# Performance work log

Measured on AMD Instinct MI355X. Metric: run time of the kernel, lower is better.

The kernel has to match this reference:

```python
import jax, jax.numpy as jnp
import numpy as np

B, N, D = 2, 2048, 512
H, VD = 8, 64  # v_dim = hid_dim / n_head


def setup_inputs() -> dict:
    key = jax.random.key(0)
    k1, k2, k3, k4 = jax.random.split(key, 4)
    inputs = jax.random.normal(k1, (B, N, D), dtype=jnp.float32)
    # lecun_normal: std = 1/sqrt(fan_in) with fan_in = D
    s = 1.0 / np.sqrt(D)
    q_w = jax.random.normal(k2, (H, D, VD), dtype=jnp.float32) * s
    k_w = jax.random.normal(k3, (H, D, VD), dtype=jnp.float32) * s
    v_w = jax.random.normal(k4, (H, D, VD), dtype=jnp.float32) * s
    return {"inputs": inputs, "q_w": q_w, "k_w": k_w, "v_w": v_w}


def reference(inputs, q_w, k_w, v_w):
    # QKV projections: [B,N,D] x [H,D,VD] -> [B,H,N,VD]
    q = jnp.einsum('bnj,hjk->bhnk', inputs, q_w)
    k = jnp.einsum('bnj,hjk->bhnk', inputs, k_w)
    v = jnp.einsum('bnj,hjk->bhnk', inputs, v_w)
    scale = 1.0 / jnp.sqrt(jnp.asarray(VD, dtype=q.dtype))
    scores = jnp.einsum('bhik,bhjk->bhij', q, k) * scale  # [B,H,N,N]
    att = jax.nn.softmax(scores, axis=-1)
    out = jnp.einsum('bhnj,bhjd->bhnd', att, v)  # [B,H,N,VD]
    out = jnp.transpose(out, (0, 2, 1, 3)).reshape(inputs.shape[0], -1, H * VD)  # [B,N,hid_dim]
    # keras GELU default is exact (non-approximate)
    return jax.nn.gelu(out, approximate=False)
```

## Files before the change

kernel.cpp:

```cpp
#include <hip/hip_runtime.h>
#include <hip/hip_bf16.h>
#include <math.h>

#define BB 2
#define NN 2048
#define DD 512
#define HH 8
#define VD 64

typedef _Float16 half8 __attribute__((ext_vector_type(8)));
typedef _Float16 half4 __attribute__((ext_vector_type(4)));
typedef __fp16 fp16x2 __attribute__((ext_vector_type(2)));
typedef float f32x4 __attribute__((ext_vector_type(4)));

#define GLDS16(gp, lp) __builtin_amdgcn_global_load_lds( \
    (const __attribute__((address_space(1))) void*)(gp), \
    (__attribute__((address_space(3))) void*)(lp), 16, 0, 0)

__device__ __forceinline__ float fexp2(float x) {
#if __has_builtin(__builtin_amdgcn_exp2f)
    return __builtin_amdgcn_exp2f(x);
#else
    return exp2f(x);
#endif
}

__device__ __forceinline__ void stage8(const _Float16* gsrc, size_t ldg, int r0,
                                       _Float16* lbase, int lane) {
    int r8 = lane >> 3;
    int ce = ((lane & 7) ^ r8) << 3;
    const _Float16* g = gsrc + (size_t)(r0 + r8) * ldg + ce;
    GLDS16(g, lbase);
}

__device__ __forceinline__ half8 frag_ld(const _Float16* tile, int row, int cb) {
    int off = row * 128 + (cb ^ ((row & 7) << 4));
    return *(const half8*)((const char*)tile + off);
}

__device__ __forceinline__ half8 frag_ldv(const _Float16* tile, int row, int cb) {
    int off = row * 256 + (cb ^ ((row & 15) << 4));
    return *(const half8*)((const char*)tile + off);
}

__device__ __forceinline__ float gelu_exact(float v) {
    return 0.5f * v * (1.f + erff(v * 0.70710678118654752f));
}

__global__ __launch_bounds__(256) void prep_kernel(
    const float* __restrict__ x,
    const float* __restrict__ qw, const float* __restrict__ kw,
    const float* __restrict__ vw,
    _Float16* __restrict__ wt, _Float16* __restrict__ xh)
{
    __shared__ float ls[64][65];
    const int t = threadIdx.x;
    const int bid = blockIdx.x;
    if (bid < 192) {
        const int kc = bid & 7, h = (bid >> 3) & 7, ty = bid >> 6;
        const float* src = (ty == 0) ? qw : (ty == 1) ? kw : vw;
#pragma unroll
        for (int j = 0; j < 4; ++j) {
            int idx = t + 256 * j;
            int k = idx >> 4, o4 = idx & 15;
            float4 v = *(const float4*)(src + ((size_t)(h * DD + kc * 64 + k) * VD + o4 * 4));
            ls[k][o4 * 4 + 0] = v.x; ls[k][o4 * 4 + 1] = v.y;
            ls[k][o4 * 4 + 2] = v.z; ls[k][o4 * 4 + 3] = v.w;
        }
        __syncthreads();
#pragma unroll
        for (int j = 0; j < 4; ++j) {
            int idx = t + 256 * j;
            int o = idx >> 4, k4 = idx & 15;
            half4 hv;
#pragma unroll
            for (int i = 0; i < 4; ++i) hv[i] = (_Float16)ls[k4 * 4 + i][o];
            *(half4*)(wt + ((size_t)(ty * HH + h) * VD + o) * DD + kc * 64 + k4 * 4) = hv;
        }
    } else {
        size_t idx = ((size_t)(bid - 192) * 256 + t) * 8;
        float4 a = *(const float4*)(x + idx);
        float4 b = *(const float4*)(x + idx + 4);
        half8 hv;
        hv[0] = (_Float16)a.x; hv[1] = (_Float16)a.y;
        hv[2] = (_Float16)a.z; hv[3] = (_Float16)a.w;
        hv[4] = (_Float16)b.x; hv[5] = (_Float16)b.y;
        hv[6] = (_Float16)b.z; hv[7] = (_Float16)b.w;
        *(half8*)(xh + idx) = hv;
    }
}

__global__ __launch_bounds__(256) void qkv_proj_kernel(
    const _Float16* __restrict__ xh,
    const _Float16* __restrict__ wt,
    _Float16* __restrict__ qsp,
    _Float16* __restrict__ kbp,
    _Float16* __restrict__ vtp)
{
    __shared__ __align__(16) _Float16 xls[2][4096];
    __shared__ __align__(16) _Float16 wls[2][12288];
    const int t = threadIdx.x;
    const int wave = t >> 6, lane = t & 63;
    const int lq = lane & 15, g = lane >> 4;
    const int bid = blockIdx.x;
    const int h = bid & 7;
    const int m0 = (bid >> 3) * 64;
    const int rbase = 32 * (wave >> 1);
    const int cbase = 96 * (wave & 1);

    f32x4 acc[2][6];
#pragma unroll
    for (int a = 0; a < 2; ++a)
#pragma unroll
        for (int c = 0; c < 6; ++c) acc[a][c] = (f32x4){0.f, 0.f, 0.f, 0.f};

    auto stage = [&](int buf, int ks) {
#pragma unroll
        for (int j = 0; j < 2; ++j) {
            int i = wave * 2 + j;
            stage8(xh + (size_t)m0 * DD + ks * 64, DD, i * 8, &xls[buf][i * 512], lane);
        }
#pragma unroll
        for (int j = 0; j < 6; ++j) {
            int i = wave * 6 + j;
            int ty = i >> 3;
            int ol = (i & 7) * 8;
            stage8(wt + ((size_t)(ty * HH + h) * VD + ol) * DD + ks * 64, DD, 0,
                   &wls[buf][i * 512], lane);
        }
    };

    stage(0, 0);
    stage(1, 1);
    for (int ks = 0; ks < 8; ++ks) {
        const int buf = ks & 1;
        if (ks < 7) asm volatile("s_waitcnt vmcnt(8)" ::: "memory");
        else        asm volatile("s_waitcnt vmcnt(0)" ::: "memory");
        __builtin_amdgcn_s_barrier();
        half8 af[2][2];
        half8 bf[6][2];
#pragma unroll
        for (int amt = 0; amt < 2; ++amt) {
            af[amt][0] = frag_ld(xls[buf], rbase + amt * 16 + lq, 16 * g);
            af[amt][1] = frag_ld(xls[buf], rbase + amt * 16 + lq, 64 + 16 * g);
        }
#pragma unroll
        for (int ct = 0; ct < 6; ++ct) {
            int wr = cbase + ct * 16 + lq;
            bf[ct][0] = frag_ld(wls[buf], wr, 16 * g);
            bf[ct][1] = frag_ld(wls[buf], wr, 64 + 16 * g);
        }
        asm volatile("s_waitcnt lgkmcnt(0)" ::: "memory");
        __builtin_amdgcn_sched_barrier(0);
        __builtin_amdgcn_s_barrier();
        if (ks + 2 < 8) stage(buf, ks + 2);
        __builtin_amdgcn_s_setprio(1);
#pragma unroll
        for (int ct = 0; ct < 6; ++ct) {
#pragma unroll
            for (int amt = 0; amt < 2; ++amt) {
                acc[amt][ct] = __builtin_amdgcn_mfma_f32_16x16x32_f16(af[amt][0], bf[ct][0], acc[amt][ct], 0, 0, 0);
                acc[amt][ct] = __builtin_amdgcn_mfma_f32_16x16x32_f16(af[amt][1], bf[ct][1], acc[amt][ct], 0, 0, 0);
            }
        }
        __builtin_amdgcn_s_setprio(0);
    }

#pragma unroll
    for (int ct = 0; ct < 6; ++ct) {
        int gcol = cbase + ct * 16 + lq;
        int ty = gcol >> 6, o = gcol & 63;
#pragma unroll
        for (int amt = 0; amt < 2; ++amt) {
#pragma unroll
            for (int i = 0; i < 4; ++i) {
                int ng = m0 + rbase + amt * 16 + 4 * g + i;
                int b = ng >> 11, nb = ng & (NN - 1);
                size_t bh = (size_t)(b * HH + h);
                float v = acc[amt][ct][i];
                if (ty == 0)      qsp[(bh * NN + nb) * VD + o] = (_Float16)(v * 0.18033688011112042f);
                else if (ty == 1) kbp[(bh * NN + nb) * VD + o] = (_Float16)v;
                else {
                    int nbp = (nb & ~31) | (((nb >> 2) & 3) << 3) | (((nb >> 4) & 1) << 2) | (nb & 3);
                    vtp[(bh * VD + o) * NN + nbp] = (_Float16)v;
                }
            }
        }
    }
}

__global__ __launch_bounds__(256, 2) void attn_kernel(
    const _Float16* __restrict__ qs,
    const _Float16* __restrict__ kb,
    const _Float16* __restrict__ vt,
    float* __restrict__ out)
{
    constexpr int NITER = NN / 128;
    __shared__ __align__(16) char SM[65536 + 1024];
    const int t = threadIdx.x;
    const int wave = t >> 6, lane = t & 63;
    const int lq = lane & 15, g = lane >> 4;
    const int bid = blockIdx.x;
    const int xcd = bid & 7;
    const int bh = xcd * 2 + ((bid >> 3) & 1);
    const int qt = bid >> 4;
    const int qbase = qt * 64;

    half8 qf[4][2];
#pragma unroll
    for (int qg = 0; qg < 4; ++qg)
#pragma unroll
        for (int ds = 0; ds < 2; ++ds)
            qf[qg][ds] = *(const half8*)(qs + ((size_t)bh * NN + qbase + 16 * qg + lq) * VD + 32 * ds + 8 * g);

    const int r8 = lane >> 3;
    const _Float16* kS = kb + ((size_t)bh * NN + 32 * wave + r8) * VD + 8 * ((lane & 7) ^ r8);
    const _Float16* vS[4];
#pragma unroll
    for (int uu = 0; uu < 4; ++uu) {
        int vrow = 16 * wave + 4 * uu + g;
        vS[uu] = vt + ((size_t)bh * VD + vrow) * NN + 8 * (lq ^ (vrow & 15));
    }

    _Float16* kb0 = (_Float16*)(SM);
    _Float16* vb0 = (_Float16*)(SM + 16384);
    _Float16* kb1 = (_Float16*)(SM + 32768);
    _Float16* vb1 = (_Float16*)(SM + 49152);

    auto stage = [&](int b, int j) {
        _Float16* kd = (b ? kb1 : kb0) + 4 * wave * 512;
        const _Float16* kp = kS + (size_t)j * 128 * VD;
#pragma unroll
        for (int uu = 0; uu < 4; ++uu)
            GLDS16(kp + uu * 8 * VD, kd + uu * 512);
        _Float16* vd = (b ? vb1 : vb0) + 4 * wave * 512;
#pragma unroll
        for (int uu = 0; uu < 4; ++uu)
            GLDS16(vS[uu] + j * 128, vd + uu * 512);
    };

    f32x4 oacc[4][4];
#pragma unroll
    for (int qg = 0; qg < 4; ++qg)
#pragma unroll
        for (int dt = 0; dt < 4; ++dt) oacc[qg][dt] = (f32x4){0.f, 0.f, 0.f, 0.f};
    float lsum[4] = {0.f, 0.f, 0.f, 0.f};

    stage(0, 0);
    stage(1, 1);

    union PU { fp16x2 h2[4]; half8 h8; };

    for (int j = 0; j < NITER; ++j) {
        const int b = j & 1;
        if (j < NITER - 1) asm volatile("s_waitcnt vmcnt(8)" ::: "memory");
        else               asm volatile("s_waitcnt vmcnt(0)" ::: "memory");
        __builtin_amdgcn_s_barrier();
        const _Float16* kB = b ? kb1 : kb0;
        const _Float16* vB = b ? vb1 : vb0;
        half8 kf[2][2], vf[4];
#pragma unroll
        for (int mt = 0; mt < 2; ++mt)
#pragma unroll
            for (int ds = 0; ds < 2; ++ds)
                kf[mt][ds] = frag_ld(kB, 32 * wave + 16 * mt + lq, 64 * ds + 16 * g);
#pragma unroll
        for (int dt = 0; dt < 4; ++dt)
            vf[dt] = frag_ldv(vB, 16 * dt + lq, 64 * wave + 16 * g);
        asm volatile("s_waitcnt lgkmcnt(0)" ::: "memory");
        __builtin_amdgcn_sched_barrier(0);
        __builtin_amdgcn_s_barrier();
        if (j + 2 < NITER) stage(b, j + 2);
        f32x4 sacc[4][2];
        __builtin_amdgcn_s_setprio(1);
#pragma unroll
        for (int qg = 0; qg < 4; ++qg) {
#pragma unroll
            for (int mt = 0; mt < 2; ++mt) {
                f32x4 sv = (f32x4){0.f, 0.f, 0.f, 0.f};
                sv = __builtin_amdgcn_mfma_f32_16x16x32_f16(kf[mt][0], qf[qg][0], sv, 0, 0, 0);
                sv = __builtin_amdgcn_mfma_f32_16x16x32_f16(kf[mt][1], qf[qg][1], sv, 0, 0, 0);
                sacc[qg][mt] = sv;
            }
        }
        __builtin_amdgcn_s_setprio(0);
        PU pu[4];
#pragma unroll
        for (int qg = 0; qg < 4; ++qg) {
            float p00 = fexp2(sacc[qg][0][0]);
            float p01 = fexp2(sacc[qg][0][1]);
            float p02 = fexp2(sacc[qg][0][2]);
            float p03 = fexp2(sacc[qg][0][3]);
            float p10 = fexp2(sacc[qg][1][0]);
            float p11 = fexp2(sacc[qg][1][1]);
            float p12 = fexp2(sacc[qg][1][2]);
            float p13 = fexp2(sacc[qg][1][3]);
            lsum[qg] += ((p00 + p01) + (p02 + p03)) + ((p10 + p11) + (p12 + p13));
            pu[qg].h2[0] = __builtin_amdgcn_cvt_pkrtz(p00, p01);
            pu[qg].h2[1] = __builtin_amdgcn_cvt_pkrtz(p02, p03);
            pu[qg].h2[2] = __builtin_amdgcn_cvt_pkrtz(p10, p11);
            pu[qg].h2[3] = __builtin_amdgcn_cvt_pkrtz(p12, p13);
        }
        __builtin_amdgcn_s_setprio(1);
#pragma unroll
        for (int qg = 0; qg < 4; ++qg)
#pragma unroll
            for (int dt = 0; dt < 4; ++dt)
                oacc[qg][dt] = __builtin_amdgcn_mfma_f32_16x16x32_f16(vf[dt], pu[qg].h8, oacc[qg][dt], 0, 0, 0);
        __builtin_amdgcn_s_setprio(0);
    }

#pragma unroll
    for (int qg = 0; qg < 4; ++qg) {
        lsum[qg] += __shfl_xor(lsum[qg], 16, 64);
        lsum[qg] += __shfl_xor(lsum[qg], 32, 64);
    }
    float* lsm  = (float*)(SM + 65536);
    float* sred = (float*)SM;
    __syncthreads();
    if (g == 0) {
#pragma unroll
        for (int qg = 0; qg < 4; ++qg) lsm[wave * 64 + 16 * qg + lq] = lsum[qg];
    }
#pragma unroll
    for (int qg = 0; qg < 4; ++qg)
#pragma unroll
        for (int dt = 0; dt < 4; ++dt)
            *(f32x4*)(sred + (size_t)wave * 4096 + (16 * qg + lq) * 64 + 16 * dt + 4 * g) = oacc[qg][dt];
    __syncthreads();
    const int b2 = bh >> 3, h = bh & 7;
    const int q = t >> 2, cg = t & 3;
    float lt = (lsm[q] + lsm[64 + q]) + (lsm[128 + q] + lsm[192 + q]);
    float inv = 1.f / lt;
    float* op = out + ((size_t)b2 * NN + qbase + q) * (HH * VD) + h * VD + 16 * cg;
#pragma unroll
    for (int c2 = 0; c2 < 4; ++c2) {
        int off = q * 64 + 16 * cg + 4 * c2;
        f32x4 o = *(const f32x4*)(sred + off);
        o += *(const f32x4*)(sred + 4096 + off);
        o += *(const f32x4*)(sred + 8192 + off);
        o += *(const f32x4*)(sred + 12288 + off);
        float4 r;
        r.x = gelu_exact(o[0] * inv);
        r.y = gelu_exact(o[1] * inv);
        r.z = gelu_exact(o[2] * inv);
        r.w = gelu_exact(o[3] * inv);
        *(float4*)(op + 4 * c2) = r;
    }
}

extern "C" void kernel_launch(void* const* d_in, const int* in_sizes, int n_in,
                              void* d_out, int out_size, void* d_ws, size_t ws_size,
                              hipStream_t stream)
{
    const float* x  = (const float*)d_in[0];
    const float* qw = (const float*)d_in[1];
    const float* kw = (const float*)d_in[2];
    const float* vw = (const float*)d_in[3];
    float* out = (float*)d_out;

    _Float16* wt  = (_Float16*)d_ws;
    _Float16* xhp = wt  + 786432;
    _Float16* qsp = xhp + 2097152;
    _Float16* kbp = qsp + 2097152;
    _Float16* vtp = kbp + 2097152;

    hipLaunchKernelGGL(prep_kernel, dim3(192 + 1024), dim3(256), 0, stream,
                       x, qw, kw, vw, wt, xhp);
    hipLaunchKernelGGL(qkv_proj_kernel, dim3(512), dim3(256), 0, stream,
                       xhp, wt, qsp, kbp, vtp);
    hipLaunchKernelGGL(attn_kernel, dim3(512), dim3(256), 0, stream,
                       qsp, kbp, vtp, out);
}
```

Measured before the change: 53.21 us.

## Enlarge QKV projection row tile and interleave score/exp/PV in attention

The QKV projection kernel now handles 128 rows per block instead of 64, halving the grid and reusing each staged weight tile across twice as many rows, at the cost of more LDS and accumulator registers. The attention loop is restructured to software-pipeline per query group: the QK^T MFMAs for the next group are issued while exp and PV run for the current group, which shortens register lifetimes and overlaps transcendental work with matrix work. The row sum of probabilities is now computed by an extra MFMA against a vector of ones instead of scalar adds and cross-lane shuffles. This adds MFMA work and a larger per-block footprint in the projection, which may reduce occupancy.

```diff
diff --git a/kernel.cpp b/kernel.cpp
--- a/kernel.cpp
+++ b/kernel.cpp
@@ -90,34 +90,34 @@
     }
 }
 
-__global__ __launch_bounds__(256) void qkv_proj_kernel(
+__global__ __launch_bounds__(256, 1) void qkv_proj_kernel(
     const _Float16* __restrict__ xh,
     const _Float16* __restrict__ wt,
     _Float16* __restrict__ qsp,
     _Float16* __restrict__ kbp,
     _Float16* __restrict__ vtp)
 {
-    __shared__ __align__(16) _Float16 xls[2][4096];
+    __shared__ __align__(16) _Float16 xls[2][8192];
     __shared__ __align__(16) _Float16 wls[2][12288];
     const int t = threadIdx.x;
     const int wave = t >> 6, lane = t & 63;
     const int lq = lane & 15, g = lane >> 4;
     const int bid = blockIdx.x;
     const int h = bid & 7;
-    const int m0 = (bid >> 3) * 64;
-    const int rbase = 32 * (wave >> 1);
+    const int m0 = (bid >> 3) * 128;
+    const int rbase = 64 * (wave >> 1);
     const int cbase = 96 * (wave & 1);
 
-    f32x4 acc[2][6];
-#pragma unroll
-    for (int a = 0; a < 2; ++a)
+    f32x4 acc[4][6];
+#pragma unroll
+    for (int a = 0; a < 4; ++a)
 #pragma unroll
         for (int c = 0; c < 6; ++c) acc[a][c] = (f32x4){0.f, 0.f, 0.f, 0.f};
 
     auto stage = [&](int buf, int ks) {
 #pragma unroll
-        for (int j = 0; j < 2; ++j) {
-            int i = wave * 2 + j;
+        for (int j = 0; j < 4; ++j) {
+            int i = wave * 4 + j;
             stage8(xh + (size_t)m0 * DD + ks * 64, DD, i * 8, &xls[buf][i * 512], lane);
         }
 #pragma unroll
@@ -134,13 +134,13 @@
     stage(1, 1);
     for (int ks = 0; ks < 8; ++ks) {
         const int buf = ks & 1;
-        if (ks < 7) asm volatile("s_waitcnt vmcnt(8)" ::: "memory");
+        if (ks < 7) asm volatile("s_waitcnt vmcnt(10)" ::: "memory");
         else        asm volatile("s_waitcnt vmcnt(0)" ::: "memory");
         __builtin_amdgcn_s_barrier();
-        half8 af[2][2];
+        half8 af[4][2];
         half8 bf[6][2];
 #pragma unroll
-        for (int amt = 0; amt < 2; ++amt) {
+        for (int amt = 0; amt < 4; ++amt) {
             af[amt][0] = frag_ld(xls[buf], rbase + amt * 16 + lq, 16 * g);
             af[amt][1] = frag_ld(xls[buf], rbase + amt * 16 + lq, 64 + 16 * g);
         }
@@ -158,7 +158,7 @@
 #pragma unroll
         for (int ct = 0; ct < 6; ++ct) {
 #pragma unroll
-            for (int amt = 0; amt < 2; ++amt) {
+            for (int amt = 0; amt < 4; ++amt) {
                 acc[amt][ct] = __builtin_amdgcn_mfma_f32_16x16x32_f16(af[amt][0], bf[ct][0], acc[amt][ct], 0, 0, 0);
                 acc[amt][ct] = __builtin_amdgcn_mfma_f32_16x16x32_f16(af[amt][1], bf[ct][1], acc[amt][ct], 0, 0, 0);
             }
@@ -171,7 +171,7 @@
         int gcol = cbase + ct * 16 + lq;
         int ty = gcol >> 6, o = gcol & 63;
 #pragma unroll
-        for (int amt = 0; amt < 2; ++amt) {
+        for (int amt = 0; amt < 4; ++amt) {
 #pragma unroll
             for (int i = 0; i < 4; ++i) {
                 int ng = m0 + rbase + amt * 16 + 4 * g + i;
@@ -240,11 +240,16 @@
     };
 
     f32x4 oacc[4][4];
-#pragma unroll
-    for (int qg = 0; qg < 4; ++qg)
+    f32x4 oacc_l[4];
+#pragma unroll
+    for (int qg = 0; qg < 4; ++qg) {
 #pragma unroll
         for (int dt = 0; dt < 4; ++dt) oacc[qg][dt] = (f32x4){0.f, 0.f, 0.f, 0.f};
-    float lsum[4] = {0.f, 0.f, 0.f, 0.f};
+        oacc_l[qg] = (f32x4){0.f, 0.f, 0.f, 0.f};
+    }
+    half8 vones;
+#pragma unroll
+    for (int i = 0; i < 8; ++i) vones[i] = (_Float16)1.0f;
 
     stage(0, 0);
     stage(1, 1);
@@ -271,56 +276,54 @@
         __builtin_amdgcn_sched_barrier(0);
         __builtin_amdgcn_s_barrier();
         if (j + 2 < NITER) stage(b, j + 2);
-        f32x4 sacc[4][2];
+        f32x4 sc[2][2];
         __builtin_amdgcn_s_setprio(1);
 #pragma unroll
+        for (int mt = 0; mt < 2; ++mt) {
+            sc[0][mt] = (f32x4){0.f, 0.f, 0.f, 0.f};
+            sc[0][mt] = __builtin_amdgcn_mfma_f32_16x16x32_f16(kf[mt][0], qf[0][0], sc[0][mt], 0, 0, 0);
+            sc[0][mt] = __builtin_amdgcn_mfma_f32_16x16x32_f16(kf[mt][1], qf[0][1], sc[0][mt], 0, 0, 0);
+        }
+#pragma unroll
         for (int qg = 0; qg < 4; ++qg) {
-#pragma unroll
-            for (int mt = 0; mt < 2; ++mt) {
-                f32x4 sv = (f32x4){0.f, 0.f, 0.f, 0.f};
-                sv = __builtin_amdgcn_mfma_f32_16x16x32_f16(kf[mt][0], qf[qg][0], sv, 0, 0, 0);
-                sv = __builtin_amdgcn_mfma_f32_16x16x32_f16(kf[mt][1], qf[qg][1], sv, 0, 0, 0);
-                sacc[qg][mt] = sv;
+            const int cur = qg & 1;
+            if (qg < 3) {
+#pragma unroll
+                for (int mt = 0; mt < 2; ++mt) {
+                    sc[cur ^ 1][mt] = (f32x4){0.f, 0.f, 0.f, 0.f};
+                    sc[cur ^ 1][mt] = __builtin_amdgcn_mfma_f32_16x16x32_f16(kf[mt][0], qf[qg + 1][0], sc[cur ^ 1][mt], 0, 0, 0);
+                    sc[cur ^ 1][mt] = __builtin_amdgcn_mfma_f32_16x16x32_f16(kf[mt][1], qf[qg + 1][1], sc[cur ^ 1][mt], 0, 0, 0);
+                }
             }
+            PU pu;
+            {
+                float p00 = fexp2(sc[cur][0][0]);
+                float p01 = fexp2(sc[cur][0][1]);
+                float p02 = fexp2(sc[cur][0][2]);
+                float p03 = fexp2(sc[cur][0][3]);
+                float p10 = fexp2(sc[cur][1][0]);
+                float p11 = fexp2(sc[cur][1][1]);
+                float p12 = fexp2(sc[cur][1][2]);
+                float p13 = fexp2(sc[cur][1][3]);
+                pu.h2[0] = __builtin_amdgcn_cvt_pkrtz(p00, p01);
+                pu.h2[1] = __builtin_amdgcn_cvt_pkrtz(p02, p03);
+                pu.h2[2] = __builtin_amdgcn_cvt_pkrtz(p10, p11);
+                pu.h2[3] = __builtin_amdgcn_cvt_pkrtz(p12, p13);
+            }
+#pragma unroll
+            for (int dt = 0; dt < 4; ++dt)
+                oacc[qg][dt] = __builtin_amdgcn_mfma_f32_16x16x32_f16(vf[dt], pu.h8, oacc[qg][dt], 0, 0, 0);
+            oacc_l[qg] = __builtin_amdgcn_mfma_f32_16x16x32_f16(vones, pu.h8, oacc_l[qg], 0, 0, 0);
         }
         __builtin_amdgcn_s_setprio(0);
-        PU pu[4];
-#pragma unroll
-        for (int qg = 0; qg < 4; ++qg) {
-            float p00 = fexp2(sacc[qg][0][0]);
-            float p01 = fexp2(sacc[qg][0][1]);
-            float p02 = fexp2(sacc[qg][0][2]);
-            float p03 = fexp2(sacc[qg][0][3]);
-            float p10 = fexp2(sacc[qg][1][0]);
-            float p11 = fexp2(sacc[qg][1][1]);
-            float p12 = fexp2(sacc[qg][1][2]);
-            float p13 = fexp2(sacc[qg][1][3]);
-            lsum[qg] += ((p00 + p01) + (p02 + p03)) + ((p10 + p11) + (p12 + p13));
-            pu[qg].h2[0] = __builtin_amdgcn_cvt_pkrtz(p00, p01);
-            pu[qg].h2[1] = __builtin_amdgcn_cvt_pkrtz(p02, p03);
-            pu[qg].h2[2] = __builtin_amdgcn_cvt_pkrtz(p10, p11);
-            pu[qg].h2[3] = __builtin_amdgcn_cvt_pkrtz(p12, p13);
-        }
-        __builtin_amdgcn_s_setprio(1);
-#pragma unroll
-        for (int qg = 0; qg < 4; ++qg)
-#pragma unroll
-            for (int dt = 0; dt < 4; ++dt)
-                oacc[qg][dt] = __builtin_amdgcn_mfma_f32_16x16x32_f16(vf[dt], pu[qg].h8, oacc[qg][dt], 0, 0, 0);
-        __builtin_amdgcn_s_setprio(0);
-    }
-
-#pragma unroll
-    for (int qg = 0; qg < 4; ++qg) {
-        lsum[qg] += __shfl_xor(lsum[qg], 16, 64);
-        lsum[qg] += __shfl_xor(lsum[qg], 32, 64);
-    }
+    }
+
     float* lsm  = (float*)(SM + 65536);
     float* sred = (float*)SM;
     __syncthreads();
     if (g == 0) {
 #pragma unroll
-        for (int qg = 0; qg < 4; ++qg) lsm[wave * 64 + 16 * qg + lq] = lsum[qg];
+        for (int qg = 0; qg < 4; ++qg) lsm[wave * 64 + 16 * qg + lq] = oacc_l[qg][0];
     }
 #pragma unroll
     for (int qg = 0; qg < 4; ++qg)
@@ -367,7 +370,7 @@
 
     hipLaunchKernelGGL(prep_kernel, dim3(192 + 1024), dim3(256), 0, stream,
                        x, qw, kw, vw, wt, xhp);
-    hipLaunchKernelGGL(qkv_proj_kernel, dim3(512), dim3(256), 0, stream,
+    hipLaunchKernelGGL(qkv_proj_kernel, dim3(256), dim3(256), 0, stream,
                        xhp, wt, qsp, kbp, vtp);
     hipLaunchKernelGGL(attn_kernel, dim3(512), dim3(256), 0, stream,
                        qsp, kbp, vtp, out);
```

New measurement: 53.36 us. Within noise of the previous version (+0.3%).
